# Performance work log

Hardware: AMD Instinct MI355X
Metric: run time of the kernel (lower is better)

Reference implementation:

```python
import jax, jax.numpy as jnp
import numpy as np

N = 100000      # nodes
E = 1600000     # edges
NODE_DIM = 128
EDGE_DIM = 32
H = 64          # hidden_dim
G = 512         # graphs in batch


def _lin(k, i, o):
    kw, kb = jax.random.split(k)
    s = 1.0 / np.sqrt(i)
    return (jax.random.uniform(kw, (i, o), jnp.float32, -s, s),
            jax.random.uniform(kb, (o,), jnp.float32, -s, s))


def setup_inputs() -> dict:
    key = jax.random.key(0)
    ks = jax.random.split(key, 12)
    x = jax.random.normal(ks[0], (N, NODE_DIM), jnp.float32)
    edge_index = jax.random.randint(ks[1], (2, E), 0, N, dtype=jnp.int64)
    edge_attr = jax.random.normal(ks[2], (E, EDGE_DIM), jnp.float32)
    batch = jnp.sort(jax.random.randint(ks[3], (N,), 0, G, dtype=jnp.int64))
    W_node, b_node = _lin(ks[4], NODE_DIM, H)
    W_edge, b_edge = _lin(ks[5], EDGE_DIM, H)
    W_g1, b_g1 = _lin(ks[6], H, H)
    W_g2, b_g2 = _lin(ks[7], H, H)
    W_g3, b_g3 = _lin(ks[8], H, H)
    W_c1, b_c1 = _lin(ks[9], H, H // 2)
    W_c2, b_c2 = _lin(ks[10], H // 2, 1)
    return dict(x=x, edge_index=edge_index, edge_attr=edge_attr, batch=batch,
                W_node=W_node, b_node=b_node, W_edge=W_edge, b_edge=b_edge,
                W_g1=W_g1, b_g1=b_g1, W_g2=W_g2, b_g2=b_g2, W_g3=W_g3, b_g3=b_g3,
                W_c1=W_c1, b_c1=b_c1, W_c2=W_c2, b_c2=b_c2)


def _gcn_norm(edge_index, n):
    # PyG gcn_norm: add self-loops, deg over targets, sym normalization
    loops = jnp.arange(n, dtype=edge_index.dtype)
    row = jnp.concatenate([edge_index[0], loops])  # source
    col = jnp.concatenate([edge_index[1], loops])  # target
    deg = jax.ops.segment_sum(jnp.ones_like(col, jnp.float32), col, num_segments=n)
    dinv = jnp.where(deg > 0, jax.lax.rsqrt(jnp.maximum(deg, 1.0)), 0.0)
    norm = dinv[row] * dinv[col]  # [E+N]
    return row, col, norm


def _gcn_conv(x, W, b, row, col, norm, n):
    h = x @ W                                           # [N,H]
    out = jax.ops.segment_sum(h[row] * norm[:, None], col, num_segments=n)
    return out + b


def reference(x, edge_index, edge_attr, batch,
              W_node, b_node, W_edge, b_edge,
              W_g1, b_g1, W_g2, b_g2, W_g3, b_g3,
              W_c1, b_c1, W_c2, b_c2):
    n = x.shape[0]
    h = x @ W_node + b_node                             # node embed [N,H]
    # edge embedding aggregated at source (index_add_ on row)
    e = edge_attr @ W_edge + b_edge                     # [E,H]
    h = h + jax.ops.segment_sum(e, edge_index[0], num_segments=n)
    # three GCNConv layers, ReLU after first two
    row, col, norm = _gcn_norm(edge_index, n)
    h = jax.nn.relu(_gcn_conv(h, W_g1, b_g1, row, col, norm, n))
    h = jax.nn.relu(_gcn_conv(h, W_g2, b_g2, row, col, norm, n))
    h = _gcn_conv(h, W_g3, b_g3, row, col, norm, n)
    # global mean pool per graph
    sums = jax.ops.segment_sum(h, batch, num_segments=G)
    cnts = jax.ops.segment_sum(jnp.ones((n,), jnp.float32), batch, num_segments=G)
    g = sums / jnp.maximum(cnts, 1.0)[:, None]          # [G,H]
    # classifier (Dropout is identity at eval)
    g = jax.nn.relu(g @ W_c1 + b_c1)
    out = g @ W_c2 + b_c2                               # [G,1]
    return out.squeeze(-1)
```

## Files before the change

### kernel.cpp

```cpp
#include <hip/hip_runtime.h>

#define NODE_DIM 128
#define HDIM 64
#define EDGE_DIM 32
#define NB 256
#define WMAX 512
#define EPB 4096

__device__ __forceinline__ void f4_add(float4& a, const float4 b) {
    a.x += b.x; a.y += b.y; a.z += b.z; a.w += b.w;
}
__device__ __forceinline__ void f4_shfl_xor_add(float4& a, int m) {
    a.x += __shfl_xor(a.x, m, 64);
    a.y += __shfl_xor(a.y, m, 64);
    a.z += __shfl_xor(a.z, m, 64);
    a.w += __shfl_xor(a.w, m, 64);
}
__device__ __forceinline__ void f4_fma(float4& a, float s, const float4 w) {
    a.x = fmaf(s, w.x, a.x); a.y = fmaf(s, w.y, a.y);
    a.z = fmaf(s, w.z, a.z); a.w = fmaf(s, w.w, a.w);
}

__global__ __launch_bounds__(256) void k_bin_count(const int* __restrict__ src,
        const int* __restrict__ dst, int* __restrict__ countD,
        int* __restrict__ countS, int E, int W) {
    __shared__ int hD[NB], hS[NB];
    int t = threadIdx.x;
    hD[t] = 0; hS[t] = 0;
    __syncthreads();
    int lo = blockIdx.x * EPB, hi = min(lo + EPB, E);
    for (int e = lo + t; e < hi; e += 256) {
        atomicAdd(&hD[dst[e] / W], 1);
        atomicAdd(&hS[src[e] / W], 1);
    }
    __syncthreads();
    if (hD[t]) atomicAdd(&countD[t], hD[t]);
    if (hS[t]) atomicAdd(&countS[t], hS[t]);
}

__global__ __launch_bounds__(256) void k_bucket_scan(const int* __restrict__ countD,
        const int* __restrict__ countS, int* __restrict__ baseD,
        int* __restrict__ baseS, int* __restrict__ curD, int* __restrict__ curS,
        int E) {
    __shared__ int tmp[NB];
    int t = threadIdx.x;
    int v = countD[t]; tmp[t] = v; __syncthreads();
    for (int off = 1; off < NB; off <<= 1) {
        int u = (t >= off) ? tmp[t - off] : 0; __syncthreads();
        tmp[t] += u; __syncthreads();
    }
    baseD[t] = tmp[t] - v; curD[t] = tmp[t] - v;
    if (t == NB - 1) baseD[NB] = E;
    __syncthreads();
    v = countS[t]; tmp[t] = v; __syncthreads();
    for (int off = 1; off < NB; off <<= 1) {
        int u = (t >= off) ? tmp[t - off] : 0; __syncthreads();
        tmp[t] += u; __syncthreads();
    }
    baseS[t] = tmp[t] - v; curS[t] = tmp[t] - v;
    if (t == NB - 1) baseS[NB] = E;
}

__global__ __launch_bounds__(256) void k_bin_scatter(const int* __restrict__ src,
        const int* __restrict__ dst, int* __restrict__ curD, int* __restrict__ curS,
        int2* __restrict__ pairD, int2* __restrict__ pairS, int E, int W) {
    __shared__ int hD[NB], hS[NB], bD[NB], bS[NB], oD[NB], oS[NB];
    int t = threadIdx.x;
    hD[t] = 0; hS[t] = 0; oD[t] = 0; oS[t] = 0;
    __syncthreads();
    int lo = blockIdx.x * EPB, hi = min(lo + EPB, E);
    for (int e = lo + t; e < hi; e += 256) {
        atomicAdd(&hD[dst[e] / W], 1);
        atomicAdd(&hS[src[e] / W], 1);
    }
    __syncthreads();
    if (hD[t]) bD[t] = atomicAdd(&curD[t], hD[t]);
    if (hS[t]) bS[t] = atomicAdd(&curS[t], hS[t]);
    __syncthreads();
    for (int e = lo + t; e < hi; e += 256) {
        int s = src[e], d = dst[e];
        int kb = d / W;
        int p = bD[kb] + atomicAdd(&oD[kb], 1);
        pairD[p] = make_int2(d, s);
        kb = s / W;
        p = bS[kb] + atomicAdd(&oS[kb], 1);
        pairS[p] = make_int2(s, e);
    }
}

__global__ __launch_bounds__(256) void k_build(const int2* __restrict__ pairs,
        const int* __restrict__ base, int* __restrict__ csr, int* __restrict__ row,
        float* __restrict__ dinv, int N, int W) {
    __shared__ int cnt[WMAX], pref[WMAX], cur[WMAX];
    int b = blockIdx.x, t = threadIdx.x;
    int nbase = b * W;
    int wlen = min(W, N - nbase);
    int pb = base[b], pe = base[b + 1];
    for (int i = t; i < W; i += 256) cnt[i] = 0;
    __syncthreads();
    for (int j = pb + t; j < pe; j += 256)
        atomicAdd(&cnt[pairs[j].x - nbase], 1);
    __syncthreads();
    if (t < 64) {
        int run = 0;
        for (int c = 0; c < W; c += 64) {
            int i = c + t;
            int v = (i < W) ? cnt[i] : 0;
            int s = v;
            for (int off = 1; off < 64; off <<= 1) {
                int u = __shfl_up(s, off, 64);
                if (t >= off) s += u;
            }
            if (i < W) pref[i] = run + s - v;
            run += __shfl(s, 63, 64);
        }
    }
    __syncthreads();
    for (int i = t; i < wlen; i += 256) {
        row[nbase + i] = pb + pref[i];
        cur[i] = pref[i];
        if (dinv) dinv[nbase + i] = 1.0f / sqrtf((float)cnt[i] + 1.0f);
    }
    if (b == gridDim.x - 1 && t == 0) row[N] = pe;
    __syncthreads();
    for (int j = pb + t; j < pe; j += 256) {
        int2 pr = pairs[j];
        int idx = atomicAdd(&cur[pr.x - nbase], 1);
        csr[pb + idx] = pr.y;
    }
}

__global__ __launch_bounds__(256) void k_foldw(const float* __restrict__ Wn,
        const float* __restrict__ We, const float* __restrict__ bn,
        const float* __restrict__ be, const float* __restrict__ W1,
        float* __restrict__ WnF, float* __restrict__ WeF,
        float* __restrict__ bnF, float* __restrict__ beF) {
    int idx = blockIdx.x * 256 + threadIdx.x;
    int row = idx >> 6, o = idx & 63;
    if (row >= NODE_DIM + EDGE_DIM + 2) return;
    const float* v; float* outp;
    if (row < NODE_DIM)                { v = Wn + row * HDIM; outp = WnF + row * HDIM; }
    else if (row < NODE_DIM + EDGE_DIM){ v = We + (row - NODE_DIM) * HDIM;
                                         outp = WeF + (row - NODE_DIM) * HDIM; }
    else if (row == NODE_DIM + EDGE_DIM){ v = bn; outp = bnF; }
    else                               { v = be; outp = beF; }
    float a = 0.f;
#pragma unroll
    for (int k = 0; k < HDIM; k++) a = fmaf(v[k], W1[k * HDIM + o], a);
    outp[o] = a;
}

__global__ __launch_bounds__(256) void k_edge_sum(const float* __restrict__ ea,
        const int* __restrict__ csr_out_e, const int* __restrict__ row_out,
        float* __restrict__ se, int n) {
    int g = threadIdx.x >> 6, lane = threadIdx.x & 63;
    int slot = lane >> 3, dq = lane & 7;
    int node = blockIdx.x * 4 + g;
    if (node >= n) return;
    int jb = row_out[node], je = row_out[node + 1];
    float4 acc = make_float4(0.f, 0.f, 0.f, 0.f);
    for (int base = jb; base < je; base += 64) {
        int cnt = min(64, je - base);
        int myidx = (base + lane < je) ? csr_out_e[base + lane] : 0;
#pragma unroll 4
        for (int t = 0; t < cnt; t += 8) {
            int which = t + slot;
            int e = __shfl(myidx, which, 64);
            if (which < cnt) {
                float4 v = *reinterpret_cast<const float4*>(
                    &ea[(size_t)e * EDGE_DIM + 4 * dq]);
                f4_add(acc, v);
            }
        }
    }
    f4_shfl_xor_add(acc, 8);
    f4_shfl_xor_add(acc, 16);
    f4_shfl_xor_add(acc, 32);
    if (slot == 0)
        *reinterpret_cast<float4*>(&se[(size_t)node * EDGE_DIM + 4 * dq]) = acc;
}

__global__ __launch_bounds__(256) void k_embed_g1t(const float* __restrict__ x,
        const float* __restrict__ se, const int* __restrict__ row_out,
        const float* __restrict__ dinv,
        const float* __restrict__ WnF, const float* __restrict__ WeF,
        const float* __restrict__ bnF, const float* __restrict__ beF,
        float* __restrict__ gout, int N) {
    __shared__ float xs[64][132];
    __shared__ float ses[64][36];
    __shared__ float dv[64], od[64];
    const int tid = threadIdx.x;
    const int node0 = blockIdx.x * 64;
    const int o0 = (tid & 7) * 8;
    const int m0 = (tid >> 3) * 2;

#pragma unroll
    for (int rep = 0; rep < 8; rep++) {
        int idx = rep * 256 + tid;
        int m = idx >> 5, c4 = (idx & 31) * 4;
        if (node0 + m < N)
            *reinterpret_cast<float4*>(&xs[m][c4]) =
                *reinterpret_cast<const float4*>(&x[(size_t)(node0 + m) * NODE_DIM + c4]);
    }
#pragma unroll
    for (int rep = 0; rep < 2; rep++) {
        int idx = rep * 256 + tid;
        int m = idx >> 3, c4 = (idx & 7) * 4;
        if (node0 + m < N)
            *reinterpret_cast<float4*>(&ses[m][c4]) =
                *reinterpret_cast<const float4*>(&se[(size_t)(node0 + m) * EDGE_DIM + c4]);
    }
    if (tid < 64) {
        int node = node0 + tid;
        if (node < N) {
            dv[tid] = dinv[node];
            od[tid] = (float)(row_out[node + 1] - row_out[node]);
        } else { dv[tid] = 0.f; od[tid] = 0.f; }
    }
    __syncthreads();

    float4 bna = *reinterpret_cast<const float4*>(&bnF[o0]);
    float4 bnb = *reinterpret_cast<const float4*>(&bnF[o0 + 4]);
    float4 bea = *reinterpret_cast<const float4*>(&beF[o0]);
    float4 beb = *reinterpret_cast<const float4*>(&beF[o0 + 4]);
    float4 acc[2][2];
#pragma unroll
    for (int i = 0; i < 2; i++) {
        float odv = od[m0 + i];
        acc[i][0] = make_float4(fmaf(odv, bea.x, bna.x), fmaf(odv, bea.y, bna.y),
                                fmaf(odv, bea.z, bna.z), fmaf(odv, bea.w, bna.w));
        acc[i][1] = make_float4(fmaf(odv, beb.x, bnb.x), fmaf(odv, beb.y, bnb.y),
                                fmaf(odv, beb.z, bnb.z), fmaf(odv, beb.w, bnb.w));
    }
    for (int k = 0; k < NODE_DIM; k += 4) {
        float4 xv0 = *reinterpret_cast<const float4*>(&xs[m0][k]);
        float4 xv1 = *reinterpret_cast<const float4*>(&xs[m0 + 1][k]);
        float x0v[4] = {xv0.x, xv0.y, xv0.z, xv0.w};
        float x1v[4] = {xv1.x, xv1.y, xv1.z, xv1.w};
#pragma unroll
        for (int j = 0; j < 4; j++) {
            float4 wa = *reinterpret_cast<const float4*>(&WnF[(k + j) * HDIM + o0]);
            float4 wb = *reinterpret_cast<const float4*>(&WnF[(k + j) * HDIM + o0 + 4]);
            f4_fma(acc[0][0], x0v[j], wa); f4_fma(acc[0][1], x0v[j], wb);
            f4_fma(acc[1][0], x1v[j], wa); f4_fma(acc[1][1], x1v[j], wb);
        }
    }
    for (int k = 0; k < EDGE_DIM; k += 4) {
        float4 sv0 = *reinterpret_cast<const float4*>(&ses[m0][k]);
        float4 sv1 = *reinterpret_cast<const float4*>(&ses[m0 + 1][k]);
        float s0v[4] = {sv0.x, sv0.y, sv0.z, sv0.w};
        float s1v[4] = {sv1.x, sv1.y, sv1.z, sv1.w};
#pragma unroll
        for (int j = 0; j < 4; j++) {
            float4 wa = *reinterpret_cast<const float4*>(&WeF[(k + j) * HDIM + o0]);
            float4 wb = *reinterpret_cast<const float4*>(&WeF[(k + j) * HDIM + o0 + 4]);
            f4_fma(acc[0][0], s0v[j], wa); f4_fma(acc[0][1], s0v[j], wb);
            f4_fma(acc[1][0], s1v[j], wa); f4_fma(acc[1][1], s1v[j], wb);
        }
    }
#pragma unroll
    for (int i = 0; i < 2; i++) {
        int node = node0 + m0 + i;
        if (node < N) {
            float d = dv[m0 + i];
            float4 r0 = acc[i][0], r1 = acc[i][1];
            r0.x *= d; r0.y *= d; r0.z *= d; r0.w *= d;
            r1.x *= d; r1.y *= d; r1.z *= d; r1.w *= d;
            *reinterpret_cast<float4*>(&gout[(size_t)node * HDIM + o0])     = r0;
            *reinterpret_cast<float4*>(&gout[(size_t)node * HDIM + o0 + 4]) = r1;
        }
    }
}

__global__ __launch_bounds__(256) void k_gather_mm(const int* __restrict__ csr_src,
        const int* __restrict__ row_in, const float* __restrict__ gbuf,
        const float* __restrict__ bin, const float* __restrict__ dinv,
        const float* __restrict__ W, float* __restrict__ gout, int n) {
    __shared__ float hs[4][HDIM];
    int g = threadIdx.x >> 6, lane = threadIdx.x & 63;
    int slot = lane >> 4, dq = lane & 15;
    int node = blockIdx.x * 4 + g;
    bool valid = node < n;
    float di = 0.f;
    float4 acc = make_float4(0.f, 0.f, 0.f, 0.f);
    if (valid) {
        di = dinv[node];
        if (slot == 0)
            acc = *reinterpret_cast<const float4*>(&gbuf[(size_t)node * HDIM + 4 * dq]);
        int jb = row_in[node], je = row_in[node + 1];
        for (int base = jb; base < je; base += 64) {
            int cnt = min(64, je - base);
            int myidx = (base + lane < je) ? csr_src[base + lane] : 0;
#pragma unroll 4
            for (int t = 0; t < cnt; t += 4) {
                int which = t + slot;
                int e = __shfl(myidx, which, 64);
                if (which < cnt) {
                    float4 v = *reinterpret_cast<const float4*>(
                        &gbuf[(size_t)e * HDIM + 4 * dq]);
                    f4_add(acc, v);
                }
            }
        }
        f4_shfl_xor_add(acc, 16);
        f4_shfl_xor_add(acc, 32);
        if (slot == 0) {
            float4 bq = *reinterpret_cast<const float4*>(&bin[4 * dq]);
            float4 z;
            z.x = fmaxf(fmaf(di, acc.x, bq.x), 0.f);
            z.y = fmaxf(fmaf(di, acc.y, bq.y), 0.f);
            z.z = fmaxf(fmaf(di, acc.z, bq.z), 0.f);
            z.w = fmaxf(fmaf(di, acc.w, bq.w), 0.f);
            *reinterpret_cast<float4*>(&hs[g][4 * dq]) = z;
        }
    }
    __syncthreads();
    if (!valid) return;
    float a = 0.f;
#pragma unroll
    for (int k = 0; k < HDIM; k++) a = fmaf(hs[g][k], W[k * HDIM + lane], a);
    gout[(size_t)node * HDIM + lane] = a * di;
}

__global__ __launch_bounds__(256) void k_gather_pool(const int* __restrict__ csr_src,
        const int* __restrict__ row_in, const float* __restrict__ gbuf,
        const float* __restrict__ bin, const float* __restrict__ dinv,
        const int* __restrict__ batch, float* __restrict__ sums,
        float* __restrict__ cnts, int n) {
    __shared__ float vs[4][HDIM];
    __shared__ int bs[4];
    int g = threadIdx.x >> 6, lane = threadIdx.x & 63;
    int slot = lane >> 4, dq = lane & 15;
    int node = blockIdx.x * 4 + g;
    bool valid = node < n;
    float di = 0.f;
    int b = -1;
    float4 acc = make_float4(0.f, 0.f, 0.f, 0.f);
    if (valid) {
        di = dinv[node];
        b = batch[node];
        if (slot == 0)
            acc = *reinterpret_cast<const float4*>(&gbuf[(size_t)node * HDIM + 4 * dq]);
        int jb = row_in[node], je = row_in[node + 1];
        for (int base = jb; base < je; base += 64) {
            int cnt = min(64, je - base);
            int myidx = (base + lane < je) ? csr_src[base + lane] : 0;
#pragma unroll 4
            for (int t = 0; t < cnt; t += 4) {
                int which = t + slot;
                int e = __shfl(myidx, which, 64);
                if (which < cnt) {
                    float4 v = *reinterpret_cast<const float4*>(
                        &gbuf[(size_t)e * HDIM + 4 * dq]);
                    f4_add(acc, v);
                }
            }
        }
        f4_shfl_xor_add(acc, 16);
        f4_shfl_xor_add(acc, 32);
        if (slot == 0) {
            float4 bq = *reinterpret_cast<const float4*>(&bin[4 * dq]);
            float4 z;
            z.x = fmaf(di, acc.x, bq.x);
            z.y = fmaf(di, acc.y, bq.y);
            z.z = fmaf(di, acc.z, bq.z);
            z.w = fmaf(di, acc.w, bq.w);
            *reinterpret_cast<float4*>(&vs[g][4 * dq]) = z;
        }
    }
    if (lane == 0) bs[g] = b;
    __syncthreads();
    bool same = (bs[0] >= 0 && bs[0] == bs[1] && bs[1] == bs[2] && bs[2] == bs[3]);
    if (same) {
        if (g == 0) {
            float t = vs[0][lane] + vs[1][lane] + vs[2][lane] + vs[3][lane];
            atomicAdd(&sums[(size_t)bs[0] * HDIM + lane], t);
            if (lane == 0) atomicAdd(&cnts[bs[0]], 4.0f);
        }
    } else if (valid) {
        atomicAdd(&sums[(size_t)b * HDIM + lane], vs[g][lane]);
        if (lane == 0) atomicAdd(&cnts[b], 1.0f);
    }
}

__global__ __launch_bounds__(64) void k_cls(const float* __restrict__ sums,
        const float* __restrict__ cnts, const float* __restrict__ W1,
        const float* __restrict__ b1, const float* __restrict__ W2,
        const float* __restrict__ b2, float* __restrict__ out) {
    __shared__ float gs[HDIM];
    __shared__ float zs[32];
    int b = blockIdx.x, t = threadIdx.x;
    float cnt = fmaxf(cnts[b], 1.0f);
    gs[t] = sums[(size_t)b * HDIM + t] / cnt;
    __syncthreads();
    if (t < 32) {
        float a = b1[t];
#pragma unroll
        for (int k = 0; k < HDIM; k++) a = fmaf(gs[k], W1[k * 32 + t], a);
        zs[t] = fmaxf(a, 0.0f);
    }
    __syncthreads();
    if (t == 0) {
        float a = b2[0];
#pragma unroll
        for (int k = 0; k < 32; k++) a = fmaf(zs[k], W2[k], a);
        out[b] = a;
    }
}

extern "C" void kernel_launch(void* const* d_in, const int* in_sizes, int n_in,
                              void* d_out, int out_size, void* d_ws, size_t ws_size,
                              hipStream_t stream) {
    const float* x      = (const float*)d_in[0];
    const int*   ei     = (const int*)d_in[1];
    const float* ea     = (const float*)d_in[2];
    const int*   batch  = (const int*)d_in[3];
    const float* W_node = (const float*)d_in[4];
    const float* b_node = (const float*)d_in[5];
    const float* W_edge = (const float*)d_in[6];
    const float* b_edge = (const float*)d_in[7];
    const float* W_g1   = (const float*)d_in[8];
    const float* b_g1   = (const float*)d_in[9];
    const float* W_g2   = (const float*)d_in[10];
    const float* b_g2   = (const float*)d_in[11];
    const float* W_g3   = (const float*)d_in[12];
    const float* b_g3   = (const float*)d_in[13];
    const float* W_c1   = (const float*)d_in[14];
    const float* b_c1   = (const float*)d_in[15];
    const float* W_c2   = (const float*)d_in[16];
    const float* b_c2   = (const float*)d_in[17];

    const int N = in_sizes[0] / NODE_DIM;
    const int E = in_sizes[2] / EDGE_DIM;
    const int G = out_size;
    const int W = (N + NB - 1) / NB;
    const int* src = ei;
    const int* dst = ei + E;

    char* ws = (char*)d_ws;
    size_t off = 0;
    auto carve = [&](size_t bytes) -> void* {
        void* p = ws + off;
        off += (bytes + 255) & ~(size_t)255;
        return p;
    };
    int*   counts     = (int*)carve((size_t)2 * NB * 4);
    int*   baseD      = (int*)carve((size_t)(NB + 1) * 4);
    int*   baseS      = (int*)carve((size_t)(NB + 1) * 4);
    int*   curD       = (int*)carve((size_t)NB * 4);
    int*   curS       = (int*)carve((size_t)NB * 4);
    int*   row_in     = (int*)carve((size_t)(N + 1) * 4);
    int*   row_out    = (int*)carve((size_t)(N + 1) * 4);
    int*   csr_in_src = (int*)carve((size_t)E * 4);
    int*   csr_out_e  = (int*)carve((size_t)E * 4);
    float* dinv       = (float*)carve((size_t)N * 4);
    float* se         = (float*)carve((size_t)N * EDGE_DIM * 4);
    float* B          = (float*)carve((size_t)N * HDIM * 4);
    float* C          = (float*)carve((size_t)N * HDIM * 4);
    float* sums       = (float*)carve((size_t)G * HDIM * 4);
    float* cnts       = (float*)carve((size_t)G * 4);
    float* WnF        = (float*)carve((size_t)NODE_DIM * HDIM * 4);
    float* WeF        = (float*)carve((size_t)EDGE_DIM * HDIM * 4);
    float* bnF        = (float*)carve((size_t)HDIM * 4);
    float* beF        = (float*)carve((size_t)HDIM * 4);
    int*   countD = counts, *countS = counts + NB;
    int2*  pairD = (int2*)B;
    int2*  pairS = (int2*)C;

    hipMemsetAsync(counts, 0, (size_t)2 * NB * 4, stream);
    hipMemsetAsync(sums, 0, (size_t)G * HDIM * 4, stream);
    hipMemsetAsync(cnts, 0, (size_t)G * 4, stream);

    const int nb_nodes = (N + 3) / 4;
    const int nb_bin   = (E + EPB - 1) / EPB;
    const int nb_t64   = (N + 63) / 64;

    k_foldw<<<((NODE_DIM + EDGE_DIM + 2) * HDIM + 255) / 256, 256, 0, stream>>>(
        W_node, W_edge, b_node, b_edge, W_g1, WnF, WeF, bnF, beF);

    k_bin_count<<<nb_bin, 256, 0, stream>>>(src, dst, countD, countS, E, W);
    k_bucket_scan<<<1, 256, 0, stream>>>(countD, countS, baseD, baseS, curD, curS, E);
    k_bin_scatter<<<nb_bin, 256, 0, stream>>>(src, dst, curD, curS, pairD, pairS, E, W);
    k_build<<<NB, 256, 0, stream>>>(pairD, baseD, csr_in_src, row_in, dinv, N, W);
    k_build<<<NB, 256, 0, stream>>>(pairS, baseS, csr_out_e, row_out, nullptr, N, W);

    k_edge_sum<<<nb_nodes, 256, 0, stream>>>(ea, csr_out_e, row_out, se, N);
    k_embed_g1t<<<nb_t64, 256, 0, stream>>>(x, se, row_out, dinv, WnF, WeF, bnF, beF,
                                            B, N);

    k_gather_mm<<<nb_nodes, 256, 0, stream>>>(csr_in_src, row_in, B, b_g1, dinv,
                                              W_g2, C, N);
    k_gather_mm<<<nb_nodes, 256, 0, stream>>>(csr_in_src, row_in, C, b_g2, dinv,
                                              W_g3, B, N);

    k_gather_pool<<<nb_nodes, 256, 0, stream>>>(csr_in_src, row_in, B, b_g3,
                                                dinv, batch, sums, cnts, N);
    k_cls<<<G, 64, 0, stream>>>(sums, cnts, W_c1, b_c1, W_c2, b_c2, (float*)d_out);
}
```

Before: 570.3 us.

## Pack bin pairs into 32-bit words, merge CSR builds, stage node weights in LDS

Result: faster. 530.3 us (-7.0%).

```diff
diff --git a/kernel.cpp b/kernel.cpp
--- a/kernel.cpp
+++ b/kernel.cpp
@@ -63,7 +63,7 @@
 
 __global__ __launch_bounds__(256) void k_bin_scatter(const int* __restrict__ src,
         const int* __restrict__ dst, int* __restrict__ curD, int* __restrict__ curS,
-        int2* __restrict__ pairD, int2* __restrict__ pairS, int E, int W) {
+        unsigned* __restrict__ pairD, unsigned* __restrict__ pairS, int E, int W) {
     __shared__ int hD[NB], hS[NB], bD[NB], bS[NB], oD[NB], oS[NB];
     int t = threadIdx.x;
     hD[t] = 0; hS[t] = 0; oD[t] = 0; oS[t] = 0;
@@ -81,25 +81,35 @@
         int s = src[e], d = dst[e];
         int kb = d / W;
         int p = bD[kb] + atomicAdd(&oD[kb], 1);
-        pairD[p] = make_int2(d, s);
+        pairD[p] = ((unsigned)(d - kb * W) << 23) | (unsigned)s;
         kb = s / W;
         p = bS[kb] + atomicAdd(&oS[kb], 1);
-        pairS[p] = make_int2(s, e);
-    }
-}
-
-__global__ __launch_bounds__(256) void k_build(const int2* __restrict__ pairs,
-        const int* __restrict__ base, int* __restrict__ csr, int* __restrict__ row,
-        float* __restrict__ dinv, int N, int W) {
+        pairS[p] = ((unsigned)(s - kb * W) << 21) | (unsigned)e;
+    }
+}
+
+__global__ __launch_bounds__(256) void k_build2(const unsigned* __restrict__ pairD,
+        const unsigned* __restrict__ pairS, const int* __restrict__ baseD,
+        const int* __restrict__ baseS, int* __restrict__ csrD,
+        int* __restrict__ csrS, int* __restrict__ rowD, int* __restrict__ rowS,
+        float* __restrict__ dinvp, int N, int W) {
     __shared__ int cnt[WMAX], pref[WMAX], cur[WMAX];
-    int b = blockIdx.x, t = threadIdx.x;
+    const int half = blockIdx.x >> 8;
+    const int b = blockIdx.x & (NB - 1);
+    const unsigned* pairs = half ? pairS : pairD;
+    const int* base = half ? baseS : baseD;
+    int* csr = half ? csrS : csrD;
+    int* row = half ? rowS : rowD;
+    const int shift = half ? 21 : 23;
+    const unsigned mask = (1u << shift) - 1u;
+    int t = threadIdx.x;
     int nbase = b * W;
     int wlen = min(W, N - nbase);
     int pb = base[b], pe = base[b + 1];
     for (int i = t; i < W; i += 256) cnt[i] = 0;
     __syncthreads();
     for (int j = pb + t; j < pe; j += 256)
-        atomicAdd(&cnt[pairs[j].x - nbase], 1);
+        atomicAdd(&cnt[pairs[j] >> shift], 1);
     __syncthreads();
     if (t < 64) {
         int run = 0;
@@ -119,14 +129,14 @@
     for (int i = t; i < wlen; i += 256) {
         row[nbase + i] = pb + pref[i];
         cur[i] = pref[i];
-        if (dinv) dinv[nbase + i] = 1.0f / sqrtf((float)cnt[i] + 1.0f);
-    }
-    if (b == gridDim.x - 1 && t == 0) row[N] = pe;
+        if (!half) dinvp[nbase + i] = 1.0f / sqrtf((float)cnt[i] + 1.0f);
+    }
+    if (b == NB - 1 && t == 0) row[N] = base[NB];
     __syncthreads();
     for (int j = pb + t; j < pe; j += 256) {
-        int2 pr = pairs[j];
-        int idx = atomicAdd(&cur[pr.x - nbase], 1);
-        csr[pb + idx] = pr.y;
+        unsigned pr = pairs[j];
+        int idx = atomicAdd(&cur[pr >> shift], 1);
+        csr[pb + idx] = (int)(pr & mask);
     }
 }
 
@@ -180,12 +190,13 @@
         *reinterpret_cast<float4*>(&se[(size_t)node * EDGE_DIM + 4 * dq]) = acc;
 }
 
-__global__ __launch_bounds__(256) void k_embed_g1t(const float* __restrict__ x,
+__global__ __launch_bounds__(256) void k_embed_g1w(const float* __restrict__ x,
         const float* __restrict__ se, const int* __restrict__ row_out,
         const float* __restrict__ dinv,
         const float* __restrict__ WnF, const float* __restrict__ WeF,
         const float* __restrict__ bnF, const float* __restrict__ beF,
         float* __restrict__ gout, int N) {
+    __shared__ float wn[NODE_DIM][HDIM];
     __shared__ float xs[64][132];
     __shared__ float ses[64][36];
     __shared__ float dv[64], od[64];
@@ -194,27 +205,33 @@
     const int o0 = (tid & 7) * 8;
     const int m0 = (tid >> 3) * 2;
 
-#pragma unroll
-    for (int rep = 0; rep < 8; rep++) {
-        int idx = rep * 256 + tid;
+    {
+        const float4* s4 = reinterpret_cast<const float4*>(WnF);
+        float4* d4 = reinterpret_cast<float4*>(&wn[0][0]);
+#pragma unroll
+        for (int r = 0; r < 8; r++) d4[r * 256 + tid] = s4[r * 256 + tid];
+    }
+#pragma unroll
+    for (int r = 0; r < 8; r++) {
+        int idx = r * 256 + tid;
         int m = idx >> 5, c4 = (idx & 31) * 4;
         if (node0 + m < N)
             *reinterpret_cast<float4*>(&xs[m][c4]) =
                 *reinterpret_cast<const float4*>(&x[(size_t)(node0 + m) * NODE_DIM + c4]);
     }
 #pragma unroll
-    for (int rep = 0; rep < 2; rep++) {
-        int idx = rep * 256 + tid;
+    for (int r = 0; r < 2; r++) {
+        int idx = r * 256 + tid;
         int m = idx >> 3, c4 = (idx & 7) * 4;
         if (node0 + m < N)
             *reinterpret_cast<float4*>(&ses[m][c4]) =
                 *reinterpret_cast<const float4*>(&se[(size_t)(node0 + m) * EDGE_DIM + c4]);
     }
     if (tid < 64) {
-        int node = node0 + tid;
-        if (node < N) {
-            dv[tid] = dinv[node];
-            od[tid] = (float)(row_out[node + 1] - row_out[node]);
+        int nd = node0 + tid;
+        if (nd < N) {
+            dv[tid] = dinv[nd];
+            od[tid] = (float)(row_out[nd + 1] - row_out[nd]);
         } else { dv[tid] = 0.f; od[tid] = 0.f; }
     }
     __syncthreads();
@@ -239,8 +256,8 @@
         float x1v[4] = {xv1.x, xv1.y, xv1.z, xv1.w};
 #pragma unroll
         for (int j = 0; j < 4; j++) {
-            float4 wa = *reinterpret_cast<const float4*>(&WnF[(k + j) * HDIM + o0]);
-            float4 wb = *reinterpret_cast<const float4*>(&WnF[(k + j) * HDIM + o0 + 4]);
+            float4 wa = *reinterpret_cast<const float4*>(&wn[k + j][o0]);
+            float4 wb = *reinterpret_cast<const float4*>(&wn[k + j][o0 + 4]);
             f4_fma(acc[0][0], x0v[j], wa); f4_fma(acc[0][1], x0v[j], wb);
             f4_fma(acc[1][0], x1v[j], wa); f4_fma(acc[1][1], x1v[j], wb);
         }
@@ -464,8 +481,8 @@
     float* bnF        = (float*)carve((size_t)HDIM * 4);
     float* beF        = (float*)carve((size_t)HDIM * 4);
     int*   countD = counts, *countS = counts + NB;
-    int2*  pairD = (int2*)B;
-    int2*  pairS = (int2*)C;
+    unsigned* pairD = (unsigned*)B;
+    unsigned* pairS = (unsigned*)C;
 
     hipMemsetAsync(counts, 0, (size_t)2 * NB * 4, stream);
     hipMemsetAsync(sums, 0, (size_t)G * HDIM * 4, stream);
@@ -481,11 +498,12 @@
     k_bin_count<<<nb_bin, 256, 0, stream>>>(src, dst, countD, countS, E, W);
     k_bucket_scan<<<1, 256, 0, stream>>>(countD, countS, baseD, baseS, curD, curS, E);
     k_bin_scatter<<<nb_bin, 256, 0, stream>>>(src, dst, curD, curS, pairD, pairS, E, W);
-    k_build<<<NB, 256, 0, stream>>>(pairD, baseD, csr_in_src, row_in, dinv, N, W);
-    k_build<<<NB, 256, 0, stream>>>(pairS, baseS, csr_out_e, row_out, nullptr, N, W);
+    k_build2<<<2 * NB, 256, 0, stream>>>(pairD, pairS, baseD, baseS,
+                                         csr_in_src, csr_out_e, row_in, row_out,
+                                         dinv, N, W);
 
     k_edge_sum<<<nb_nodes, 256, 0, stream>>>(ea, csr_out_e, row_out, se, N);
-    k_embed_g1t<<<nb_t64, 256, 0, stream>>>(x, se, row_out, dinv, WnF, WeF, bnF, beF,
+    k_embed_g1w<<<nb_t64, 256, 0, stream>>>(x, se, row_out, dinv, WnF, WeF, bnF, beF,
                                             B, N);
 
     k_gather_mm<<<nb_nodes, 256, 0, stream>>>(csr_in_src, row_in, B, b_g1, dinv,
```
